# Performance work log

Measured on AMD Instinct MI355X. Metric: run time of the kernel, lower is better.

## Reference

```python
import jax, jax.numpy as jnp
import numpy as np

B, N, F = 8, 500000, 1000000


def setup_inputs() -> dict:
    key = jax.random.key(0)
    k1, k2 = jax.random.split(key)
    vert = jax.random.normal(k1, (B, N, 3), dtype=jnp.float32)
    faces = jax.random.randint(k2, (F, 3), 0, N, dtype=jnp.int64)
    return {"vert": vert, "faces": faces}


def _uniform_laplacian(vert, faces):
    # vert: [B, N, 3], faces: [F, 3]
    n = vert.shape[1]
    i, j, k = faces[:, 0], faces[:, 1], faces[:, 2]
    # 6 directed edges per face: dst accumulates its neighbors' positions (src)
    dst = jnp.concatenate([i, i, j, j, k, k])  # [6F]
    src = jnp.concatenate([j, k, i, k, i, j])  # [6F]
    deg = jax.ops.segment_sum(jnp.ones_like(dst, dtype=vert.dtype), dst, num_segments=n)  # [N]
    nbr_sum = jax.vmap(lambda v: jax.ops.segment_sum(v[src], dst, num_segments=n))(vert)  # [B,N,3]
    # lap = mean(neighbors) - v  (uniform Laplacian: D^{-1} A - I)
    return nbr_sum / jnp.maximum(deg, 1.0)[None, :, None] - vert


def reference(vert, faces):
    lap = _uniform_laplacian(vert, faces)          # [B, N, 3]
    curve = jnp.sqrt(jnp.sum(lap * lap, axis=-1))  # [B, N] (L2 norm over xyz)
    return curve
```

## Files before the change

kernel.cpp:

```cpp
#include <hip/hip_runtime.h>
#include <hip/hip_fp16.h>
#include <math.h>

#define BATCH 8
#define NBUK_MAX 512
#define BSHIFT 10
#define CAPB 6656
#define PACK_MASK 0x7FFFFull
#define SCAN_T 256
#define SCAN_E 8
#define SCAN_TILE (SCAN_T * SCAN_E)

union H2U { __half2 h; unsigned u; };

__device__ __forceinline__ long long pack3(int v, int a, int b) {
    return (long long)(((unsigned long long)(unsigned)v) |
                       ((unsigned long long)(unsigned)a << 19) |
                       ((unsigned long long)(unsigned)b << 38));
}

__global__ __launch_bounds__(1024) void expand_repack_kernel(
        const int* __restrict__ faces,
        int* __restrict__ cursor,
        long long* __restrict__ recbuf,
        const float* __restrict__ vert,
        uint2* __restrict__ vh,
        int N, int F, int expBlocks) {
    if ((int)blockIdx.x < expBlocks) {
        __shared__ int hist[NBUK_MAX];
        __shared__ int sbuf[NBUK_MAX];
        __shared__ int lbase[NBUK_MAX];
        __shared__ int gb[NBUK_MAX];
        __shared__ long long stage[3072];
        int tid = threadIdx.x;
        for (int x = tid; x < NBUK_MAX; x += 1024) hist[x] = 0;
        __syncthreads();

        int f = blockIdx.x * 1024 + tid;
        bool valid = f < F;
        int bb0 = 0, bb1 = 0, bb2 = 0, rr0 = 0, rr1 = 0, rr2 = 0;
        long long rc0 = 0, rc1 = 0, rc2 = 0;
        if (valid) {
            int i = faces[3 * f + 0];
            int j = faces[3 * f + 1];
            int k = faces[3 * f + 2];
            rc0 = pack3(i, j, k);
            rc1 = pack3(j, i, k);
            rc2 = pack3(k, i, j);
            bb0 = i >> BSHIFT; bb1 = j >> BSHIFT; bb2 = k >> BSHIFT;
            rr0 = atomicAdd(&hist[bb0], 1);
            rr1 = atomicAdd(&hist[bb1], 1);
            rr2 = atomicAdd(&hist[bb2], 1);
        }
        __syncthreads();

        if (tid < NBUK_MAX) sbuf[tid] = hist[tid];
        __syncthreads();
        for (int d = 1; d < NBUK_MAX; d <<= 1) {
            int t = 0;
            if (tid < NBUK_MAX && tid >= d) t = sbuf[tid - d];
            __syncthreads();
            if (tid < NBUK_MAX) sbuf[tid] += t;
            __syncthreads();
        }
        if (tid < NBUK_MAX) {
            lbase[tid] = sbuf[tid] - hist[tid];
            gb[tid] = (hist[tid] > 0) ? atomicAdd(&cursor[tid * 16], hist[tid]) : 0;
        }
        __syncthreads();

        if (valid) {
            stage[lbase[bb0] + rr0] = rc0;
            stage[lbase[bb1] + rr1] = rc1;
            stage[lbase[bb2] + rr2] = rc2;
        }
        __syncthreads();

        int total = sbuf[NBUK_MAX - 1];
        for (int t = tid; t < total; t += 1024) {
            long long r = stage[t];
            int v = (int)((unsigned long long)r & PACK_MASK);
            int b = v >> BSHIFT;
            int gpos = gb[b] + (t - lbase[b]);
            if (gpos < CAPB)
                recbuf[(size_t)b * CAPB + gpos] = r;
        }
    } else {
        int u = (blockIdx.x - expBlocks) * 1024 + threadIdx.x;
        if (u < N * BATCH) {
            int v = u >> 3;
            int b = u & 7;
            size_t src = ((size_t)b * N + v) * 3;
            H2U xy, zw;
            xy.h = __floats2half2_rn(vert[src], vert[src + 1]);
            zw.h = __floats2half2_rn(vert[src + 2], 0.0f);
            uint2 w; w.x = xy.u; w.y = zw.u;
            vh[u] = w;
        }
    }
}

__device__ __forceinline__ void unpack_acc(uint2 r, float& ax, float& ay, float& az) {
    H2U xy, zw; xy.u = r.x; zw.u = r.y;
    float2 f0 = __half22float2(xy.h);
    float2 f1 = __half22float2(zw.h);
    ax += f0.x; ay += f0.y; az += f1.x;
}

__global__ __launch_bounds__(1024) void bucket_gather_kernel(
        const int* __restrict__ cursor,
        const long long* __restrict__ recbuf,
        const uint2* __restrict__ vh,
        float* __restrict__ out, int N) {
    __shared__ int cntL[1024];
    __shared__ int offL[1024];
    __shared__ int2 colbuf[CAPB];
    int tid = threadIdx.x;
    int bid = blockIdx.x;
    int v0 = bid << BSHIFT;

    int rc = cursor[bid * 16];
    int rcnt = rc < CAPB ? rc : CAPB;

    cntL[tid] = 0;
    __syncthreads();
    const long long* recs = recbuf + (size_t)bid * CAPB;
    for (int x = tid; x < rcnt; x += 1024) {
        int v = (int)((unsigned long long)recs[x] & PACK_MASK);
        atomicAdd(&cntL[v & 1023], 2);
    }
    __syncthreads();

    int myc = cntL[tid];
    for (int d = 1; d < 1024; d <<= 1) {
        int t = (tid >= d) ? cntL[tid - d] : 0;
        __syncthreads();
        cntL[tid] += t;
        __syncthreads();
    }
    int myoff = cntL[tid] - myc;
    cntL[tid] = myoff;
    offL[tid] = myoff;
    __syncthreads();

    for (int x = tid; x < rcnt; x += 1024) {
        unsigned long long r = (unsigned long long)recs[x];
        int v = (int)(r & PACK_MASK);
        int a = (int)((r >> 19) & PACK_MASK);
        int b = (int)((r >> 38) & PACK_MASK);
        int p = atomicAdd(&cntL[v & 1023], 2);
        colbuf[p >> 1] = make_int2(a, b);
    }
    __syncthreads();

    int b = tid & 7;
    for (int it = 0; it < (1 << BSHIFT) / 128; ++it) {
        int lv = (tid >> 3) + 128 * it;
        int v = v0 + lv;
        if (v >= N) continue;
        int start = offL[lv];
        int end = cntL[lv];
        int c = end - start;
        int e = start >> 1, e1 = end >> 1;

        float ax = 0.f, ay = 0.f, az = 0.f;
        for (; e + 4 <= e1; e += 4) {
            int2 s01 = colbuf[e];
            int2 s23 = colbuf[e + 1];
            int2 s45 = colbuf[e + 2];
            int2 s67 = colbuf[e + 3];
            uint2 r0 = vh[((size_t)s01.x << 3) + b];
            uint2 r1 = vh[((size_t)s01.y << 3) + b];
            uint2 r2 = vh[((size_t)s23.x << 3) + b];
            uint2 r3 = vh[((size_t)s23.y << 3) + b];
            uint2 r4 = vh[((size_t)s45.x << 3) + b];
            uint2 r5 = vh[((size_t)s45.y << 3) + b];
            uint2 r6 = vh[((size_t)s67.x << 3) + b];
            uint2 r7 = vh[((size_t)s67.y << 3) + b];
            unpack_acc(r0, ax, ay, az); unpack_acc(r1, ax, ay, az);
            unpack_acc(r2, ax, ay, az); unpack_acc(r3, ax, ay, az);
            unpack_acc(r4, ax, ay, az); unpack_acc(r5, ax, ay, az);
            unpack_acc(r6, ax, ay, az); unpack_acc(r7, ax, ay, az);
        }
        for (; e < e1; ++e) {
            int2 ss = colbuf[e];
            uint2 r0 = vh[((size_t)ss.x << 3) + b];
            uint2 r1 = vh[((size_t)ss.y << 3) + b];
            unpack_acc(r0, ax, ay, az);
            unpack_acc(r1, ax, ay, az);
        }

        float invd = 1.0f / fmaxf((float)c, 1.0f);
        float sx = 0.f, sy = 0.f, sz = 0.f;
        unpack_acc(vh[((size_t)v << 3) + b], sx, sy, sz);
        float l0 = ax * invd - sx;
        float l1 = ay * invd - sy;
        float l2 = az * invd - sz;
        out[(size_t)b * N + v] = sqrtf(l0 * l0 + l1 * l1 + l2 * l2);
    }
}


__global__ void count_only_kernel(const int* __restrict__ faces, int* __restrict__ cnt,
                                  int* __restrict__ rank, int F) {
    int f = blockIdx.x * blockDim.x + threadIdx.x;
    if (f >= F) return;
    rank[3 * f + 0] = atomicAdd(&cnt[faces[3 * f + 0]], 2);
    rank[3 * f + 1] = atomicAdd(&cnt[faces[3 * f + 1]], 2);
    rank[3 * f + 2] = atomicAdd(&cnt[faces[3 * f + 2]], 2);
}

__global__ void scan_sums_kernel(const int* __restrict__ cnt, int* __restrict__ bsums, int N) {
    __shared__ int sh[SCAN_T];
    int base = blockIdx.x * SCAN_TILE + threadIdx.x * SCAN_E;
    int s = 0;
    #pragma unroll
    for (int e = 0; e < SCAN_E; ++e)
        if (base + e < N) s += cnt[base + e];
    sh[threadIdx.x] = s;
    __syncthreads();
    for (int d = SCAN_T / 2; d > 0; d >>= 1) {
        if (threadIdx.x < (unsigned)d) sh[threadIdx.x] += sh[threadIdx.x + d];
        __syncthreads();
    }
    if (threadIdx.x == 0) bsums[blockIdx.x] = sh[0];
}

__global__ void scan_apply_kernel(const int* __restrict__ cnt, int* __restrict__ off,
                                  const int* __restrict__ bsums, int N, int nb) {
    __shared__ int shb[SCAN_T];
    __shared__ int sh[SCAN_T];
    int bv = ((int)threadIdx.x < nb) ? bsums[threadIdx.x] : 0;
    shb[threadIdx.x] = bv;
    __syncthreads();
    for (int d = 1; d < SCAN_T; d <<= 1) {
        int t = (threadIdx.x >= (unsigned)d) ? shb[threadIdx.x - d] : 0;
        __syncthreads();
        shb[threadIdx.x] += t;
        __syncthreads();
    }
    int block_prefix = (blockIdx.x > 0) ? shb[blockIdx.x - 1] : 0;

    int base = blockIdx.x * SCAN_TILE + threadIdx.x * SCAN_E;
    int vals[SCAN_E];
    int s = 0;
    #pragma unroll
    for (int e = 0; e < SCAN_E; ++e) {
        int v = (base + e < N) ? cnt[base + e] : 0;
        vals[e] = v; s += v;
    }
    sh[threadIdx.x] = s;
    __syncthreads();
    for (int d = 1; d < SCAN_T; d <<= 1) {
        int t = (threadIdx.x >= (unsigned)d) ? sh[threadIdx.x - d] : 0;
        __syncthreads();
        sh[threadIdx.x] += t;
        __syncthreads();
    }
    int excl = block_prefix + ((threadIdx.x > 0) ? sh[threadIdx.x - 1] : 0);
    #pragma unroll
    for (int e = 0; e < SCAN_E; ++e) {
        if (base + e < N) off[base + e] = excl;
        excl += vals[e];
    }
}

__global__ void fill_kernel(const int* __restrict__ faces, const int* __restrict__ off,
                            const int* __restrict__ rank, int* __restrict__ col, int F) {
    int f = blockIdx.x * blockDim.x + threadIdx.x;
    if (f >= F) return;
    int i = faces[3 * f + 0];
    int j = faces[3 * f + 1];
    int k = faces[3 * f + 2];
    int2* c2 = (int2*)col;
    c2[(off[i] + rank[3 * f + 0]) >> 1] = make_int2(j, k);
    c2[(off[j] + rank[3 * f + 1]) >> 1] = make_int2(i, k);
    c2[(off[k] + rank[3 * f + 2]) >> 1] = make_int2(i, j);
}

__global__ void gather_scalar_kernel(const float* __restrict__ vert,
                                     const int* __restrict__ cnt,
                                     const int* __restrict__ off,
                                     const int* __restrict__ col,
                                     float* __restrict__ out, int N) {
    int v = blockIdx.x * blockDim.x + threadIdx.x;
    if (v >= N) return;
    int c = cnt[v];
    int start = off[v];
    int end = start + c;
    float ax[BATCH], ay[BATCH], az[BATCH];
    #pragma unroll
    for (int b = 0; b < BATCH; ++b) { ax[b] = 0.f; ay[b] = 0.f; az[b] = 0.f; }
    for (int e = start; e < end; ++e) {
        int s = col[e];
        #pragma unroll
        for (int b = 0; b < BATCH; ++b) {
            size_t base = ((size_t)b * N + s) * 3;
            ax[b] += vert[base + 0];
            ay[b] += vert[base + 1];
            az[b] += vert[base + 2];
        }
    }
    float invd = 1.0f / fmaxf((float)c, 1.0f);
    #pragma unroll
    for (int b = 0; b < BATCH; ++b) {
        size_t base = ((size_t)b * N + v) * 3;
        float l0 = ax[b] * invd - vert[base + 0];
        float l1 = ay[b] * invd - vert[base + 1];
        float l2 = az[b] * invd - vert[base + 2];
        out[(size_t)b * N + v] = sqrtf(l0 * l0 + l1 * l1 + l2 * l2);
    }
}


static inline size_t align256(size_t x) { return (x + 255) & ~(size_t)255; }

extern "C" void kernel_launch(void* const* d_in, const int* in_sizes, int n_in,
                              void* d_out, int out_size, void* d_ws, size_t ws_size,
                              hipStream_t stream) {
    const float* vert  = (const float*)d_in[0];
    const int*   faces = (const int*)d_in[1];
    float*       out   = (float*)d_out;

    int N = out_size / BATCH;
    int F = in_sizes[1] / 3;
    int E = 6 * F;
    int NB = (N + (1 << BSHIFT) - 1) >> BSHIFT;

    char* ws = (char*)d_ws;

    size_t o_cursor = 0;
    size_t o_vh     = NBUK_MAX * 64;
    size_t o_rec    = o_vh + align256((size_t)N * BATCH * sizeof(uint2));
    size_t need     = o_rec + (size_t)NB * CAPB * 8;

    if (ws_size >= need && N <= 524288 && NB <= NBUK_MAX) {
        int*       cursor = (int*)(ws + o_cursor);
        uint2*     vh     = (uint2*)(ws + o_vh);
        long long* rec    = (long long*)(ws + o_rec);

        (void)hipMemsetAsync(cursor, 0, NBUK_MAX * 64, stream);

        int expB = (F + 1023) / 1024;
        int repB = (N * BATCH + 1023) / 1024;
        expand_repack_kernel<<<expB + repB, 1024, 0, stream>>>(
            faces, cursor, rec, vert, vh, N, F, expB);

        bucket_gather_kernel<<<NB, 1024, 0, stream>>>(cursor, rec, vh, out, N);
        return;
    }

    int threads = 256;
    int nb = (N + SCAN_TILE - 1) / SCAN_TILE;
    size_t f_cnt   = 0;
    size_t f_off   = align256((size_t)N * 4);
    size_t f_bsums = f_off + align256((size_t)N * 4);
    size_t f_col   = f_bsums + 4096;
    size_t f_rank  = f_col + align256((size_t)E * 4);

    int* cnt   = (int*)(ws + f_cnt);
    int* off   = (int*)(ws + f_off);
    int* bsums = (int*)(ws + f_bsums);
    int* col   = (int*)(ws + f_col);
    int* rank  = (int*)(ws + f_rank);

    (void)hipMemsetAsync(cnt, 0, (size_t)N * 4, stream);

    int cntBlocks = (F + threads - 1) / threads;
    count_only_kernel<<<cntBlocks, threads, 0, stream>>>(faces, cnt, rank, F);
    scan_sums_kernel<<<nb, SCAN_T, 0, stream>>>(cnt, bsums, N);
    scan_apply_kernel<<<nb, SCAN_T, 0, stream>>>(cnt, off, bsums, N, nb);
    fill_kernel<<<cntBlocks, threads, 0, stream>>>(faces, off, rank, col, F);
    gather_scalar_kernel<<<(N + threads - 1) / threads, threads, 0, stream>>>(
        vert, cnt, off, col, out, N);
}
```

Before: 236.5 us.

## Split expand and repack kernels, process four faces per thread, drop LDS staging

The fused expand/repack kernel becomes two launches. The expand kernel now handles 4096 faces per block, which amortises each global cursor atomic over more records. It also writes records straight to their bucket slot instead of staging them in shared memory and running a 512-wide block scan. This cuts global atomics and barriers, but the global writes are less coalesced, and the extra launch serialises work that used to overlap in one grid.

```diff
diff --git a/kernel.cpp b/kernel.cpp
--- a/kernel.cpp
+++ b/kernel.cpp
@@ -7,6 +7,9 @@
 #define BSHIFT 10
 #define CAPB 6656
 #define PACK_MASK 0x7FFFFull
+#define EXP_T 1024
+#define EXP_Q 4
+#define EXP_FACES (EXP_T * EXP_Q)
 #define SCAN_T 256
 #define SCAN_E 8
 #define SCAN_TILE (SCAN_T * SCAN_E)
@@ -19,84 +22,79 @@
                        ((unsigned long long)(unsigned)b << 38));
 }
 
-__global__ __launch_bounds__(1024) void expand_repack_kernel(
+__global__ __launch_bounds__(EXP_T) void expand_kernel(
         const int* __restrict__ faces,
         int* __restrict__ cursor,
         long long* __restrict__ recbuf,
+        int F) {
+    __shared__ int hist[NBUK_MAX];
+    __shared__ int gb[NBUK_MAX];
+    int tid = threadIdx.x;
+    if (tid < NBUK_MAX) hist[tid] = 0;
+    __syncthreads();
+
+    int fbase = blockIdx.x * EXP_FACES;
+    int idx[EXP_Q][3];
+    bool val[EXP_Q];
+    #pragma unroll
+    for (int q = 0; q < EXP_Q; ++q) {
+        int f = fbase + q * EXP_T + tid;
+        val[q] = f < F;
+        if (val[q]) {
+            idx[q][0] = faces[3 * f + 0];
+            idx[q][1] = faces[3 * f + 1];
+            idx[q][2] = faces[3 * f + 2];
+        } else {
+            idx[q][0] = 0; idx[q][1] = 0; idx[q][2] = 0;
+        }
+    }
+
+    int rr[EXP_Q][3];
+    #pragma unroll
+    for (int q = 0; q < EXP_Q; ++q) {
+        if (val[q]) {
+            rr[q][0] = atomicAdd(&hist[idx[q][0] >> BSHIFT], 1);
+            rr[q][1] = atomicAdd(&hist[idx[q][1] >> BSHIFT], 1);
+            rr[q][2] = atomicAdd(&hist[idx[q][2] >> BSHIFT], 1);
+        }
+    }
+    __syncthreads();
+
+    if (tid < NBUK_MAX) {
+        int h = hist[tid];
+        gb[tid] = (h > 0) ? atomicAdd(&cursor[tid * 16], h) : 0;
+    }
+    __syncthreads();
+
+    #pragma unroll
+    for (int q = 0; q < EXP_Q; ++q) {
+        if (val[q]) {
+            int i = idx[q][0], j = idx[q][1], k = idx[q][2];
+            int b0 = i >> BSHIFT, b1 = j >> BSHIFT, b2 = k >> BSHIFT;
+            int p0 = gb[b0] + rr[q][0];
+            int p1 = gb[b1] + rr[q][1];
+            int p2 = gb[b2] + rr[q][2];
+            if (p0 < CAPB) recbuf[(size_t)b0 * CAPB + p0] = pack3(i, j, k);
+            if (p1 < CAPB) recbuf[(size_t)b1 * CAPB + p1] = pack3(j, i, k);
+            if (p2 < CAPB) recbuf[(size_t)b2 * CAPB + p2] = pack3(k, i, j);
+        }
+    }
+}
+
+__global__ __launch_bounds__(1024) void repack_kernel(
         const float* __restrict__ vert,
         uint2* __restrict__ vh,
-        int N, int F, int expBlocks) {
-    if ((int)blockIdx.x < expBlocks) {
-        __shared__ int hist[NBUK_MAX];
-        __shared__ int sbuf[NBUK_MAX];
-        __shared__ int lbase[NBUK_MAX];
-        __shared__ int gb[NBUK_MAX];
-        __shared__ long long stage[3072];
-        int tid = threadIdx.x;
-        for (int x = tid; x < NBUK_MAX; x += 1024) hist[x] = 0;
-        __syncthreads();
-
-        int f = blockIdx.x * 1024 + tid;
-        bool valid = f < F;
-        int bb0 = 0, bb1 = 0, bb2 = 0, rr0 = 0, rr1 = 0, rr2 = 0;
-        long long rc0 = 0, rc1 = 0, rc2 = 0;
-        if (valid) {
-            int i = faces[3 * f + 0];
-            int j = faces[3 * f + 1];
-            int k = faces[3 * f + 2];
-            rc0 = pack3(i, j, k);
-            rc1 = pack3(j, i, k);
-            rc2 = pack3(k, i, j);
-            bb0 = i >> BSHIFT; bb1 = j >> BSHIFT; bb2 = k >> BSHIFT;
-            rr0 = atomicAdd(&hist[bb0], 1);
-            rr1 = atomicAdd(&hist[bb1], 1);
-            rr2 = atomicAdd(&hist[bb2], 1);
-        }
-        __syncthreads();
-
-        if (tid < NBUK_MAX) sbuf[tid] = hist[tid];
-        __syncthreads();
-        for (int d = 1; d < NBUK_MAX; d <<= 1) {
-            int t = 0;
-            if (tid < NBUK_MAX && tid >= d) t = sbuf[tid - d];
-            __syncthreads();
-            if (tid < NBUK_MAX) sbuf[tid] += t;
-            __syncthreads();
-        }
-        if (tid < NBUK_MAX) {
-            lbase[tid] = sbuf[tid] - hist[tid];
-            gb[tid] = (hist[tid] > 0) ? atomicAdd(&cursor[tid * 16], hist[tid]) : 0;
-        }
-        __syncthreads();
-
-        if (valid) {
-            stage[lbase[bb0] + rr0] = rc0;
-            stage[lbase[bb1] + rr1] = rc1;
-            stage[lbase[bb2] + rr2] = rc2;
-        }
-        __syncthreads();
-
-        int total = sbuf[NBUK_MAX - 1];
-        for (int t = tid; t < total; t += 1024) {
-            long long r = stage[t];
-            int v = (int)((unsigned long long)r & PACK_MASK);
-            int b = v >> BSHIFT;
-            int gpos = gb[b] + (t - lbase[b]);
-            if (gpos < CAPB)
-                recbuf[(size_t)b * CAPB + gpos] = r;
-        }
-    } else {
-        int u = (blockIdx.x - expBlocks) * 1024 + threadIdx.x;
-        if (u < N * BATCH) {
-            int v = u >> 3;
-            int b = u & 7;
-            size_t src = ((size_t)b * N + v) * 3;
-            H2U xy, zw;
-            xy.h = __floats2half2_rn(vert[src], vert[src + 1]);
-            zw.h = __floats2half2_rn(vert[src + 2], 0.0f);
-            uint2 w; w.x = xy.u; w.y = zw.u;
-            vh[u] = w;
-        }
+        int N) {
+    int u = blockIdx.x * 1024 + threadIdx.x;
+    if (u < N * BATCH) {
+        int v = u >> 3;
+        int b = u & 7;
+        size_t src = ((size_t)b * N + v) * 3;
+        H2U xy, zw;
+        xy.h = __floats2half2_rn(vert[src], vert[src + 1]);
+        zw.h = __floats2half2_rn(vert[src + 2], 0.0f);
+        uint2 w; w.x = xy.u; w.y = zw.u;
+        vh[u] = w;
     }
 }
 
@@ -341,11 +339,10 @@
 
         (void)hipMemsetAsync(cursor, 0, NBUK_MAX * 64, stream);
 
-        int expB = (F + 1023) / 1024;
+        int expB = (F + EXP_FACES - 1) / EXP_FACES;
         int repB = (N * BATCH + 1023) / 1024;
-        expand_repack_kernel<<<expB + repB, 1024, 0, stream>>>(
-            faces, cursor, rec, vert, vh, N, F, expB);
-
+        expand_kernel<<<expB, EXP_T, 0, stream>>>(faces, cursor, rec, F);
+        repack_kernel<<<repB, 1024, 0, stream>>>(vert, vh, N);
         bucket_gather_kernel<<<NB, 1024, 0, stream>>>(cursor, rec, vh, out, N);
         return;
     }
```

New measurement: 231.8 us. 2.0% less time.
